# Kernel tuning notes

Measured on AMD Instinct MI355X. Metric: run time of the kernel, lower is better.

The kernel has to match this reference:

```python
import jax, jax.numpy as jnp
import numpy as np

B, T, D, H, BAND = 2, 4096, 512, 8, 16
LN_EPS = 1e-5


def setup_inputs() -> dict:
    key = jax.random.key(0)
    k0, k1, k2 = jax.random.split(key, 3)
    x = jax.random.normal(k0, (B, T, D), jnp.float32)
    # nn.MultiheadAttention params: packed in_proj [3D, D] and out_proj [D, D]
    w_in = jax.random.normal(k1, (3 * D, D), jnp.float32) * 0.02
    b_in = jnp.zeros((3 * D,), jnp.float32)
    w_out = jax.random.normal(k2, (D, D), jnp.float32) * 0.02
    b_out = jnp.zeros((D,), jnp.float32)
    ln_g = jnp.ones((D,), jnp.float32)
    ln_b = jnp.zeros((D,), jnp.float32)
    return dict(x=x, ln_g=ln_g, ln_b=ln_b, w_in=w_in, b_in=b_in,
                w_out=w_out, b_out=b_out)


def reference(x, ln_g, ln_b, w_in, b_in, w_out, b_out):
    Bq, Tq, Dq = x.shape
    dh = Dq // H
    # LayerNorm
    mu = jnp.mean(x, axis=-1, keepdims=True)
    var = jnp.mean(jnp.square(x - mu), axis=-1, keepdims=True)
    h = (x - mu) * jax.lax.rsqrt(var + LN_EPS) * ln_g + ln_b
    # packed QKV projection (torch Linear: y = h @ W^T + b)
    qkv = h @ w_in.T + b_in                      # [B, T, 3D]
    q, k, v = jnp.split(qkv, 3, axis=-1)
    to_heads = lambda a: a.reshape(Bq, Tq, H, dh).transpose(0, 2, 1, 3)  # [B,H,T,dh]
    q, k, v = to_heads(q), to_heads(k), to_heads(v)
    # band-gather: each query t attends to keys in [t-BAND, t+BAND]
    Wn = 2 * BAND + 1
    offs = jnp.arange(-BAND, BAND + 1)
    idx = jnp.arange(Tq)[:, None] + offs[None, :]          # [T, Wn]
    valid = (idx >= 0) & (idx < Tq)                        # [T, Wn]
    idx_c = jnp.clip(idx, 0, Tq - 1)
    k_win = k[:, :, idx_c]                                 # [B,H,T,Wn,dh]
    v_win = v[:, :, idx_c]                                 # [B,H,T,Wn,dh]
    scale = 1.0 / np.sqrt(dh).astype(np.float32)
    scores = jnp.einsum('bhtd,bhtwd->bhtw', q * scale, k_win)
    scores = jnp.where(valid[None, None], scores, -jnp.inf)
    p = jax.nn.softmax(scores, axis=-1)                    # [B,H,T,Wn]
    o = jnp.einsum('bhtw,bhtwd->bhtd', p, v_win)           # [B,H,T,dh]
    o = o.transpose(0, 2, 1, 3).reshape(Bq, Tq, Dq)
    y = o @ w_out.T + b_out
    return x + y
```

## Files before the change

kernel.cpp:

```cpp
#include <hip/hip_runtime.h>
#include <hip/hip_bf16.h>

#define T_ 4096
#define D_ 512
#define H_ 8
#define BAND 16
#define G1_K 512

typedef float f32x4 __attribute__((ext_vector_type(4)));
typedef __bf16 bf16x8 __attribute__((ext_vector_type(8)));
typedef unsigned short us8 __attribute__((ext_vector_type(8)));
typedef unsigned short us4 __attribute__((ext_vector_type(4)));

__device__ __forceinline__ unsigned short f2b(float f) {
  union { float f; unsigned u; } v; v.f = f;
  unsigned r = v.u + 0x7fffu + ((v.u >> 16) & 1u);
  return (unsigned short)(r >> 16);
}

__device__ __forceinline__ f32x4 mfma16(bf16x8 a, bf16x8 b, f32x4 c) {
  return __builtin_amdgcn_mfma_f32_16x16x32_bf16(a, b, c, 0, 0, 0);
}

#define GLD16(gp, lp) __builtin_amdgcn_global_load_lds( \
    (const __attribute__((address_space(1))) void*)(gp), \
    (__attribute__((address_space(3))) void*)(lp), 16, 0, 0)

__global__ __launch_bounds__(256) void prep_k(const float* __restrict__ x,
                                              const float* __restrict__ g,
                                              const float* __restrict__ bt,
                                              const float* __restrict__ win,
                                              const float* __restrict__ wout,
                                              unsigned short* __restrict__ h,
                                              unsigned short* __restrict__ winb,
                                              unsigned short* __restrict__ woutb) {
  int bx = blockIdx.x;
  if (bx >= 2048) {
    int i = (bx - 2048) * 256 + threadIdx.x;
    const int n1 = 3 * D_ * D_ / 4;
    if (i < n1) {
      float4 v = ((const float4*)win)[i];
      us4 o; o.x = f2b(v.x); o.y = f2b(v.y); o.z = f2b(v.z); o.w = f2b(v.w);
      ((us4*)winb)[i] = o;
    } else {
      int j = i - n1;
      float4 v = ((const float4*)wout)[j];
      us4 o; o.x = f2b(v.x); o.y = f2b(v.y); o.z = f2b(v.z); o.w = f2b(v.w);
      ((us4*)woutb)[j] = o;
    }
    return;
  }
  int wave = threadIdx.x >> 6, lane = threadIdx.x & 63;
  size_t row = (size_t)bx * 4 + wave;
  const float4* xr = (const float4*)(x + row * D_);
  float4 a = xr[lane * 2], b = xr[lane * 2 + 1];
  float s = a.x + a.y + a.z + a.w + b.x + b.y + b.z + b.w;
  #pragma unroll
  for (int o = 32; o; o >>= 1) s += __shfl_xor(s, o, 64);
  float mu = s * (1.0f / D_);
  float d0 = a.x - mu, d1 = a.y - mu, d2 = a.z - mu, d3 = a.w - mu;
  float d4 = b.x - mu, d5 = b.y - mu, d6 = b.z - mu, d7 = b.w - mu;
  float q = d0*d0 + d1*d1 + d2*d2 + d3*d3 + d4*d4 + d5*d5 + d6*d6 + d7*d7;
  #pragma unroll
  for (int o = 32; o; o >>= 1) q += __shfl_xor(q, o, 64);
  float rstd = rsqrtf(q * (1.0f / D_) + 1e-5f);
  const float4* gr = (const float4*)g;
  const float4* br = (const float4*)bt;
  float4 g0 = gr[lane * 2], g1 = gr[lane * 2 + 1];
  float4 b0 = br[lane * 2], b1 = br[lane * 2 + 1];
  us8 o8;
  o8[0] = f2b(d0 * rstd * g0.x + b0.x);
  o8[1] = f2b(d1 * rstd * g0.y + b0.y);
  o8[2] = f2b(d2 * rstd * g0.z + b0.z);
  o8[3] = f2b(d3 * rstd * g0.w + b0.w);
  o8[4] = f2b(d4 * rstd * g1.x + b1.x);
  o8[5] = f2b(d5 * rstd * g1.y + b1.y);
  o8[6] = f2b(d6 * rstd * g1.z + b1.z);
  o8[7] = f2b(d7 * rstd * g1.w + b1.w);
  *((us8*)(h + row * D_) + lane) = o8;
}

#define SLOT_SZ 28672

__device__ __forceinline__ void stgA(const unsigned short* __restrict__ gb,
                                     unsigned short* lds, int slot, int h, int tt,
                                     int rl0, int u0, int su) {
  #pragma unroll
  for (int j = 0; j < 2; ++j) {
    int row = h * 128 + rl0 + 64 * j;
    GLD16(gb + (size_t)row * G1_K + tt * 64 + su, lds + slot * SLOT_SZ + row * 64 + u0 * 8);
  }
}
__device__ __forceinline__ void stgB(const unsigned short* __restrict__ gb,
                                     unsigned short* lds, int slot, int tt,
                                     int rl0, int u0, int su) {
  #pragma unroll
  for (int c = 0; c < 3; ++c) {
    int row = c * 64 + rl0;
    GLD16(gb + (size_t)row * G1_K + tt * 64 + su, lds + slot * SLOT_SZ + 16384 + row * 64 + u0 * 8);
  }
}

#define VMC3 asm volatile("s_waitcnt vmcnt(3)" ::: "memory")
#define VMC0 asm volatile("s_waitcnt vmcnt(0)" ::: "memory")

#define PHASE(SLOT, PH, STAGE_STMT, WAIT_STMT) do {                                        \
    if ((PH) == 0) {                                                                       \
      _Pragma("unroll") for (int nf = 0; nf < 3; ++nf) {                                   \
        breg[nf][0] = *(const bf16x8*)(lds + (SLOT)*SLOT_SZ + boff + nf*1024 + swz0);      \
        breg[nf][1] = *(const bf16x8*)(lds + (SLOT)*SLOT_SZ + boff + nf*1024 + swz1);      \
      }                                                                                    \
    }                                                                                      \
    bf16x8 a0k0 = *(const bf16x8*)(lds + (SLOT)*SLOT_SZ + aoff + (2*(PH))*1024 + swz0);    \
    bf16x8 a0k1 = *(const bf16x8*)(lds + (SLOT)*SLOT_SZ + aoff + (2*(PH))*1024 + swz1);    \
    bf16x8 a1k0 = *(const bf16x8*)(lds + (SLOT)*SLOT_SZ + aoff + (2*(PH)+1)*1024 + swz0);  \
    bf16x8 a1k1 = *(const bf16x8*)(lds + (SLOT)*SLOT_SZ + aoff + (2*(PH)+1)*1024 + swz1);  \
    STAGE_STMT;                                                                            \
    __builtin_amdgcn_s_barrier();                                                          \
    asm volatile("s_waitcnt lgkmcnt(0)" ::: "memory");                                     \
    __builtin_amdgcn_sched_barrier(0);                                                     \
    __builtin_amdgcn_s_setprio(1);                                                         \
    _Pragma("unroll") for (int nf = 0; nf < 3; ++nf) {                                     \
      acc[2*(PH)][nf]   = mfma16(a0k0, breg[nf][0], acc[2*(PH)][nf]);                      \
      acc[2*(PH)][nf]   = mfma16(a0k1, breg[nf][1], acc[2*(PH)][nf]);                      \
      acc[2*(PH)+1][nf] = mfma16(a1k0, breg[nf][0], acc[2*(PH)+1][nf]);                    \
      acc[2*(PH)+1][nf] = mfma16(a1k1, breg[nf][1], acc[2*(PH)+1][nf]);                    \
    }                                                                                      \
    __builtin_amdgcn_s_setprio(0);                                                         \
    __builtin_amdgcn_sched_barrier(0);                                                     \
    WAIT_STMT;                                                                             \
    __builtin_amdgcn_s_barrier();                                                          \
  } while (0)

__global__ __launch_bounds__(512, 2) void gemm_qkv8(const unsigned short* __restrict__ A,
                                                    const unsigned short* __restrict__ Bw,
                                                    const float* __restrict__ bias,
                                                    unsigned short* __restrict__ C) {
  extern __shared__ char smem[];
  unsigned short* lds = (unsigned short*)smem;
  int tid = threadIdx.x;
  int lane = tid & 63, wave = tid >> 6;
  int wm = wave >> 2, wn = wave & 3;
  int fr = lane & 15, fq = lane >> 4;
  int d = blockIdx.x;
  int l = (d & 7) * 32 + (d >> 3);
  int bm = l >> 3, bn = l & 7;

  const unsigned short* Ag = A + (size_t)bm * 256 * G1_K;
  const unsigned short* Bg = Bw + (size_t)bn * 192 * G1_K;

  int rl0 = tid >> 3, u0 = tid & 7;
  int su = (u0 ^ (rl0 & 7)) * 8;

  int aoff = wm * 8192 + fr * 64;
  int boff = 16384 + (wn * 48 + fr) * 64;
  int swz0 = (fq ^ (fr & 7)) * 8;
  int swz1 = ((4 + fq) ^ (fr & 7)) * 8;

  f32x4 acc[8][3] = {};
  bf16x8 breg[3][2];

  stgB(Bg, lds, 0, 0, rl0, u0, su);
  stgA(Ag, lds, 0, 0, 0, rl0, u0, su);
  stgA(Ag, lds, 0, 1, 0, rl0, u0, su);
  stgB(Bg, lds, 1, 1, rl0, u0, su);
  VMC3;
  __builtin_amdgcn_s_barrier();

  #pragma unroll 1
  for (int i = 0; i < 3; ++i) {
    int t = 2 * i;
    PHASE(0, 0, stgA(Ag, lds, 1, 0, t + 1, rl0, u0, su), (void)0);
    PHASE(0, 1, stgA(Ag, lds, 1, 1, t + 1, rl0, u0, su), (void)0);
    PHASE(0, 2, stgB(Bg, lds, 0, t + 2, rl0, u0, su), (void)0);
    PHASE(0, 3, (void)0, VMC3);
    PHASE(1, 0, stgA(Ag, lds, 0, 0, t + 2, rl0, u0, su), (void)0);
    PHASE(1, 1, stgA(Ag, lds, 0, 1, t + 2, rl0, u0, su), (void)0);
    PHASE(1, 2, stgB(Bg, lds, 1, t + 3, rl0, u0, su), (void)0);
    PHASE(1, 3, (void)0, VMC3);
  }
  PHASE(0, 0, stgA(Ag, lds, 1, 0, 7, rl0, u0, su), (void)0);
  PHASE(0, 1, stgA(Ag, lds, 1, 1, 7, rl0, u0, su), (void)0);
  PHASE(0, 2, (void)0, (void)0);
  PHASE(0, 3, (void)0, VMC0);
  PHASE(1, 0, (void)0, (void)0);
  PHASE(1, 1, (void)0, (void)0);
  PHASE(1, 2, (void)0, (void)0);
  PHASE(1, 3, (void)0, (void)0);

  int rbase = bm * 256 + wm * 128 + fq * 4;
  int cbase = bn * 192 + wn * 48 + fr;
  float bv[3];
  #pragma unroll
  for (int nf = 0; nf < 3; ++nf) bv[nf] = bias[cbase + nf * 16];
  #pragma unroll
  for (int mf = 0; mf < 8; ++mf)
    #pragma unroll
    for (int nf = 0; nf < 3; ++nf)
      #pragma unroll
      for (int r = 0; r < 4; ++r)
        C[(size_t)(rbase + mf * 16 + r) * 1536 + cbase + nf * 16] = f2b(acc[mf][nf][r] + bv[nf]);
}

__global__ __launch_bounds__(256) void gemm_bt2(const unsigned short* __restrict__ A,
                                                const unsigned short* __restrict__ Bw,
                                                const float* __restrict__ bias,
                                                const float* __restrict__ xres,
                                                float* __restrict__ ofp,
                                                int N, int K) {
  __shared__ unsigned short As[128 * 64];
  __shared__ unsigned short Bs[128 * 64];
  int tid = threadIdx.x;
  int lane = tid & 63;
  int wave = tid >> 6;
  int wm = wave >> 1, wn = wave & 1;
  int fr = lane & 15, fq = lane >> 4;
  int dd = blockIdx.x;
  int nbn = N >> 7;
  int l = (dd & 7) * (gridDim.x >> 3) + (dd >> 3);
  int bm = l / nbn, bn = l % nbn;

  const unsigned short* Ap[4];
  const unsigned short* Bp[4];
  int loff[4];
  #pragma unroll
  for (int g = 0; g < 4; ++g) {
    int s = g * 256 + tid;
    int row = s >> 3, u = s & 7;
    int uu = u ^ (row & 7);
    Ap[g] = A + (size_t)(bm * 128 + row) * K + uu * 8;
    Bp[g] = Bw + (size_t)(bn * 128 + row) * K + uu * 8;
    loff[g] = s * 16;
  }

  f32x4 acc[4][4] = {};

  int nk = K >> 6;
  for (int kt = 0; kt < nk; ++kt) {
    int ko = kt * 64;
    #pragma unroll
    for (int g = 0; g < 4; ++g) GLD16(Ap[g] + ko, (char*)As + loff[g]);
    #pragma unroll
    for (int g = 0; g < 4; ++g) GLD16(Bp[g] + ko, (char*)Bs + loff[g]);
    __syncthreads();
    #pragma unroll
    for (int kk = 0; kk < 2; ++kk) {
      bf16x8 af[4], bfr[4];
      #pragma unroll
      for (int i = 0; i < 4; ++i) {
        int row = wm * 64 + i * 16 + fr;
        af[i] = *(const bf16x8*)(As + row * 64 + (((kk * 4 + fq) ^ (fr & 7)) << 3));
      }
      #pragma unroll
      for (int j = 0; j < 4; ++j) {
        int row = wn * 64 + j * 16 + fr;
        bfr[j] = *(const bf16x8*)(Bs + row * 64 + (((kk * 4 + fq) ^ (fr & 7)) << 3));
      }
      #pragma unroll
      for (int i = 0; i < 4; ++i)
        #pragma unroll
        for (int j = 0; j < 4; ++j)
          acc[i][j] = mfma16(af[i], bfr[j], acc[i][j]);
    }
    __syncthreads();
  }

  int rbase = bm * 128 + wm * 64 + fq * 4;
  int cb = bn * 128 + wn * 64 + fr;
  #pragma unroll
  for (int j = 0; j < 4; ++j) {
    int col = cb + j * 16;
    float bvv = bias[col];
    #pragma unroll
    for (int i = 0; i < 4; ++i) {
      #pragma unroll
      for (int r = 0; r < 4; ++r) {
        size_t idx = (size_t)(rbase + i * 16 + r) * N + col;
        ofp[idx] = xres[idx] + acc[i][j][r] + bvv;
      }
    }
  }
}

__global__ __launch_bounds__(256, 4) void attn_k(const unsigned short* __restrict__ qkv,
                                                 unsigned short* __restrict__ obuf) {
  __shared__ unsigned short Ks[96 * 72];
  __shared__ unsigned short Vt[64 * 104];
  __shared__ unsigned short Ps[64 * 104];
  int tid = threadIdx.x;
  int lane = tid & 63, wave = tid >> 6;
  int fr = lane & 15, fq = lane >> 4;
  int t0 = blockIdx.x * 64;
  int hh = blockIdx.y;
  int bb = blockIdx.z;
  size_t rowbase = (size_t)bb * T_;

  #pragma unroll
  for (int it = 0; it < 3; ++it) {
    int c = tid + it * 256;
    int r = c >> 3;
    int u = c & 7;
    int d8 = u * 8;
    int tg = t0 - BAND + r;
    us8 kv = {0,0,0,0,0,0,0,0}, vv = {0,0,0,0,0,0,0,0};
    if (tg >= 0 && tg < T_) {
      const unsigned short* p = qkv + (rowbase + tg) * 1536 + hh * 64 + d8;
      kv = *(const us8*)(p + 512);
      vv = *(const us8*)(p + 1024);
    }
    *(us8*)(Ks + r * 72 + d8) = kv;
    #pragma unroll
    for (int j = 0; j < 8; ++j) Vt[(d8 + j) * 104 + r] = vv[j];
  }

  bf16x8 qf0, qf1;
  {
    int tq = t0 + wave * 16 + fr;
    const unsigned short* qp = qkv + (rowbase + tq) * 1536 + hh * 64 + fq * 8;
    qf0 = *(const bf16x8*)qp;
    qf1 = *(const bf16x8*)(qp + 32);
  }
  __syncthreads();

  f32x4 sa[6];
  #pragma unroll
  for (int c = 0; c < 6; ++c) sa[c] = (f32x4){0.f, 0.f, 0.f, 0.f};
  #pragma unroll
  for (int c = 0; c < 6; ++c) {
    bf16x8 k0 = *(const bf16x8*)(Ks + (c * 16 + fr) * 72 + fq * 8);
    bf16x8 k1 = *(const bf16x8*)(Ks + (c * 16 + fr) * 72 + 32 + fq * 8);
    sa[c] = mfma16(qf0, k0, sa[c]);
    sa[c] = mfma16(qf1, k1, sa[c]);
  }

  float inv[4];
  float pvv[6][4];
  #pragma unroll
  for (int r = 0; r < 4; ++r) {
    int tg = t0 + wave * 16 + fq * 4 + r;
    float m = -1e30f;
    #pragma unroll
    for (int c = 0; c < 6; ++c) {
      int cg = t0 - BAND + c * 16 + fr;
      bool ok = (cg >= tg - BAND) && (cg <= tg + BAND) && (cg >= 0) && (cg < T_);
      float v = ok ? sa[c][r] * 0.125f : -1e30f;
      pvv[c][r] = v;
      m = fmaxf(m, v);
    }
    #pragma unroll
    for (int o = 8; o; o >>= 1) m = fmaxf(m, __shfl_xor(m, o, 64));
    float s = 0.0f;
    #pragma unroll
    for (int c = 0; c < 6; ++c) {
      float e = exp2f((pvv[c][r] - m) * 1.44269504f);
      pvv[c][r] = e;
      s += e;
    }
    #pragma unroll
    for (int o = 8; o; o >>= 1) s += __shfl_xor(s, o, 64);
    inv[r] = 1.0f / s;
  }

  #pragma unroll
  for (int c = 0; c < 6; ++c)
    #pragma unroll
    for (int r = 0; r < 4; ++r)
      Ps[(wave * 16 + fq * 4 + r) * 104 + c * 16 + fr] = f2b(pvv[c][r]);

  __syncthreads();

  f32x4 oa[4];
  #pragma unroll
  for (int c2 = 0; c2 < 4; ++c2) oa[c2] = (f32x4){0.f, 0.f, 0.f, 0.f};
  #pragma unroll
  for (int kk = 0; kk < 3; ++kk) {
    bf16x8 pa = *(const bf16x8*)(Ps + (wave * 16 + fr) * 104 + kk * 32 + fq * 8);
    #pragma unroll
    for (int c2 = 0; c2 < 4; ++c2) {
      bf16x8 vb = *(const bf16x8*)(Vt + (c2 * 16 + fr) * 104 + kk * 32 + fq * 8);
      oa[c2] = mfma16(pa, vb, oa[c2]);
    }
  }

  size_t orow = rowbase + t0 + wave * 16 + fq * 4;
  #pragma unroll
  for (int c2 = 0; c2 < 4; ++c2)
    #pragma unroll
    for (int r = 0; r < 4; ++r)
      obuf[(orow + r) * D_ + hh * 64 + c2 * 16 + fr] = f2b(oa[c2][r] * inv[r]);
}

extern "C" void kernel_launch(void* const* d_in, const int* in_sizes, int n_in,
                              void* d_out, int out_size, void* d_ws, size_t ws_size,
                              hipStream_t stream) {
  (void)in_sizes; (void)n_in; (void)out_size; (void)ws_size;
  const float* x     = (const float*)d_in[0];
  const float* ln_g  = (const float*)d_in[1];
  const float* ln_b  = (const float*)d_in[2];
  const float* w_in  = (const float*)d_in[3];
  const float* b_in  = (const float*)d_in[4];
  const float* w_out = (const float*)d_in[5];
  const float* b_out = (const float*)d_in[6];
  float* out = (float*)d_out;

  char* ws = (char*)d_ws;
  unsigned short* hb    = (unsigned short*)(ws);
  unsigned short* winb  = (unsigned short*)(ws + 8388608);
  unsigned short* woutb = (unsigned short*)(ws + 9961472);
  unsigned short* qkvb  = (unsigned short*)(ws + 10485760);
  unsigned short* obf   = (unsigned short*)(ws + 35651584);

  (void)hipFuncSetAttribute((const void*)gemm_qkv8,
                            hipFuncAttributeMaxDynamicSharedMemorySize, 114688);

  prep_k<<<3072, 256, 0, stream>>>(x, ln_g, ln_b, w_in, w_out, hb, winb, woutb);
  gemm_qkv8<<<256, 512, 114688, stream>>>(hb, winb, b_in, qkvb);
  attn_k<<<dim3(64, 8, 2), 256, 0, stream>>>(qkvb, obf);
  gemm_bt2<<<256, 256, 0, stream>>>(obf, woutb, b_out, x, out, 512, 512);
}
```

Measured before the change: 56.62 us.

## Double-buffer output-projection GEMM with async LDS prefetch two tiles ahead

Converts the output-projection GEMM from a single-buffered load-sync-compute loop to a two-slot LDS ring. The next K tiles are prefetched with global_load_lds while MFMAs run, and vmcnt waits replace full syncthreads. The aim is to hide global load latency behind compute, at the cost of doubled LDS use. The loop now assumes K=512 (8 tiles are hardcoded), which drops generality for other K values.

```diff
diff --git a/kernel.cpp b/kernel.cpp
--- a/kernel.cpp
+++ b/kernel.cpp
@@ -101,6 +101,7 @@
   }
 }
 
+#define VMC8 asm volatile("s_waitcnt vmcnt(8)" ::: "memory")
 #define VMC3 asm volatile("s_waitcnt vmcnt(3)" ::: "memory")
 #define VMC0 asm volatile("s_waitcnt vmcnt(0)" ::: "memory")
 
@@ -208,8 +209,8 @@
                                                 const float* __restrict__ xres,
                                                 float* __restrict__ ofp,
                                                 int N, int K) {
-  __shared__ unsigned short As[128 * 64];
-  __shared__ unsigned short Bs[128 * 64];
+  __shared__ unsigned short As[2 * 128 * 64];
+  __shared__ unsigned short Bs[2 * 128 * 64];
   int tid = threadIdx.x;
   int lane = tid & 63;
   int wave = tid >> 6;
@@ -235,34 +236,65 @@
 
   f32x4 acc[4][4] = {};
 
-  int nk = K >> 6;
-  for (int kt = 0; kt < nk; ++kt) {
-    int ko = kt * 64;
-    #pragma unroll
-    for (int g = 0; g < 4; ++g) GLD16(Ap[g] + ko, (char*)As + loff[g]);
-    #pragma unroll
-    for (int g = 0; g < 4; ++g) GLD16(Bp[g] + ko, (char*)Bs + loff[g]);
-    __syncthreads();
-    #pragma unroll
-    for (int kk = 0; kk < 2; ++kk) {
-      bf16x8 af[4], bfr[4];
-      #pragma unroll
-      for (int i = 0; i < 4; ++i) {
-        int row = wm * 64 + i * 16 + fr;
-        af[i] = *(const bf16x8*)(As + row * 64 + (((kk * 4 + fq) ^ (fr & 7)) << 3));
-      }
-      #pragma unroll
-      for (int j = 0; j < 4; ++j) {
-        int row = wn * 64 + j * 16 + fr;
-        bfr[j] = *(const bf16x8*)(Bs + row * 64 + (((kk * 4 + fq) ^ (fr & 7)) << 3));
-      }
-      #pragma unroll
-      for (int i = 0; i < 4; ++i)
-        #pragma unroll
-        for (int j = 0; j < 4; ++j)
-          acc[i][j] = mfma16(af[i], bfr[j], acc[i][j]);
-    }
-    __syncthreads();
+  #pragma unroll
+  for (int g = 0; g < 4; ++g) GLD16(Ap[g], (char*)As + loff[g]);
+  #pragma unroll
+  for (int g = 0; g < 4; ++g) GLD16(Bp[g], (char*)Bs + loff[g]);
+  #pragma unroll
+  for (int g = 0; g < 4; ++g) GLD16(Ap[g] + 64, (char*)As + 16384 + loff[g]);
+  #pragma unroll
+  for (int g = 0; g < 4; ++g) GLD16(Bp[g] + 64, (char*)Bs + 16384 + loff[g]);
+  VMC8;
+  __builtin_amdgcn_s_barrier();
+
+  #pragma unroll 1
+  for (int kt = 0; kt < 8; ++kt) {
+    int sl = (kt & 1) * 8192;
+    bf16x8 af[4], bfr[4];
+    #pragma unroll
+    for (int i2 = 0; i2 < 4; ++i2) {
+      int row = wm * 64 + i2 * 16 + fr;
+      af[i2] = *(const bf16x8*)(As + sl + row * 64 + ((fq ^ (fr & 7)) << 3));
+    }
+    #pragma unroll
+    for (int j = 0; j < 4; ++j) {
+      int row = wn * 64 + j * 16 + fr;
+      bfr[j] = *(const bf16x8*)(Bs + sl + row * 64 + ((fq ^ (fr & 7)) << 3));
+    }
+    #pragma unroll
+    for (int i2 = 0; i2 < 4; ++i2)
+      #pragma unroll
+      for (int j = 0; j < 4; ++j)
+        acc[i2][j] = mfma16(af[i2], bfr[j], acc[i2][j]);
+    bf16x8 af1[4], bfr1[4];
+    #pragma unroll
+    for (int i2 = 0; i2 < 4; ++i2) {
+      int row = wm * 64 + i2 * 16 + fr;
+      af1[i2] = *(const bf16x8*)(As + sl + row * 64 + (((4 + fq) ^ (fr & 7)) << 3));
+    }
+    #pragma unroll
+    for (int j = 0; j < 4; ++j) {
+      int row = wn * 64 + j * 16 + fr;
+      bfr1[j] = *(const bf16x8*)(Bs + sl + row * 64 + (((4 + fq) ^ (fr & 7)) << 3));
+    }
+    asm volatile("s_waitcnt lgkmcnt(0)" ::: "memory");
+    __builtin_amdgcn_sched_barrier(0);
+    __builtin_amdgcn_s_barrier();
+    if (kt < 6) {
+      int ko = (kt + 2) * 64;
+      #pragma unroll
+      for (int g = 0; g < 4; ++g) GLD16(Ap[g] + ko, (char*)As + (sl << 1) + loff[g]);
+      #pragma unroll
+      for (int g = 0; g < 4; ++g) GLD16(Bp[g] + ko, (char*)Bs + (sl << 1) + loff[g]);
+    }
+    #pragma unroll
+    for (int i2 = 0; i2 < 4; ++i2)
+      #pragma unroll
+      for (int j = 0; j < 4; ++j)
+        acc[i2][j] = mfma16(af1[i2], bfr1[j], acc[i2][j]);
+    if (kt < 6)      { VMC8; }
+    else if (kt == 6){ VMC0; }
+    __builtin_amdgcn_s_barrier();
   }
 
   int rbase = bm * 128 + wm * 64 + fq * 4;
@@ -272,11 +304,11 @@
     int col = cb + j * 16;
     float bvv = bias[col];
     #pragma unroll
-    for (int i = 0; i < 4; ++i) {
+    for (int i2 = 0; i2 < 4; ++i2) {
       #pragma unroll
       for (int r = 0; r < 4; ++r) {
-        size_t idx = (size_t)(rbase + i * 16 + r) * N + col;
-        ofp[idx] = xres[idx] + acc[i][j][r] + bvv;
+        size_t idx = (size_t)(rbase + i2 * 16 + r) * N + col;
+        ofp[idx] = xres[idx] + acc[i2][j][r] + bvv;
       }
     }
   }
```

Result: no change. 55.54 us (-1.9%).
